# Optimization experiments

Measured on AMD Instinct MI355X. Metric: run time of the kernel, lower is better.

## Reference

```python
import jax, jax.numpy as jnp
import numpy as np

N_E = 1024      # nconcepts (codebook size)
E_DIM = 64      # cdim (codebook vector dim)
BETA = 0.25
LEGACY = True


def setup_inputs() -> dict:
    key = jax.random.key(0)
    k1, k2, k3 = jax.random.split(key, 3)
    z_ = jax.random.normal(k1, (32, 256, 32, 32), jnp.float32)
    # 1x1 conv dis_modulator: 256 -> 64 channels (stored as [out, in])
    conv_w = jax.random.normal(k2, (64, 256), jnp.float32) / np.sqrt(256.0)
    conv_b = jnp.zeros((64,), jnp.float32)
    # embedding.weight.data.uniform_(-1/n_e, 1/n_e)
    emb = jax.random.uniform(k3, (N_E, E_DIM), jnp.float32, -1.0 / N_E, 1.0 / N_E)
    return {"z_": z_, "conv_w": conv_w, "conv_b": conv_b, "emb": emb}


def _forward(z_, conv_w, conv_b, emb):
    sg = jax.lax.stop_gradient
    # dis_modulator: 1x1 conv == per-pixel linear map  (B,Cin,H,W)->(B,Cout,H,W)
    z = jnp.einsum('bchw,oc->bohw', z_, conv_w) + conv_b[None, :, None, None]
    B = z.shape[0]
    # torch .view(-1, e_dim): row-major flatten of (B,C,H,W) into chunks of e_dim
    zf = z.reshape(-1, E_DIM)  # [B*C*H*W/e_dim, e_dim]

    # contrastive term: mean pairwise cosine similarity of codebook rows
    d1 = emb @ emb.T                                  # [n_e, n_e]
    norms = jnp.linalg.norm(emb, axis=1)              # [n_e]
    cosine = d1 / (norms[:, None] * norms[None, :])
    contrastive = jnp.mean(cosine)

    # squared L2 distances: ||z||^2 + ||e||^2 - 2 z.e
    d = (jnp.sum(zf * zf, axis=1, keepdims=True)
         + jnp.sum(emb * emb, axis=1)[None, :]
         - 2.0 * (zf @ emb.T))                        # [N, n_e]
    idx = jnp.argmin(d, axis=1)                       # [N]
    z_q = emb[idx].reshape(z.shape)

    if LEGACY:
        loss = jnp.mean((sg(z_q) - z) ** 2) + BETA * jnp.mean((z_q - sg(z)) ** 2)
    else:
        loss = BETA * jnp.mean((sg(z_q) - z) ** 2) + jnp.mean((z_q - sg(z)) ** 2)
    # hessian_penalty(G, z_, G_z=z): G is an affine 1x1 conv, so the central
    # second difference G(z+x) - 2G(z) + G(z-x) is identically zero -> penalty = 0.
    loss = loss + contrastive

    # straight-through estimator
    z_q_st = z + sg(z_q - z)

    # replicate source exactly: flat zeros(B*n_e) scattered at codebook indices
    sampled = jnp.zeros((B * N_E,), z.dtype).at[idx].set(1.0).reshape(B, N_E)
    min_idx = idx.reshape(B, -1)
    return z_q_st, loss, sampled, min_idx


def reference(z_, conv_w, conv_b, emb):
    z_q, loss, sampled, min_idx = _forward(z_, conv_w, conv_b, emb)
    return z_q, loss, sampled, min_idx
```

## Files before the change

### kernel.cpp

```cpp
#include <hip/hip_runtime.h>
#include <hip/hip_bf16.h>

#define BATCH   32
#define CIN     256
#define COUT    64
#define HW      1024
#define NE      1024
#define ED      64
#define NROW    32768
#define ZTOT    2097152

#define OFF_LOSS 2097152
#define OFF_SAMP 2097153
#define OFF_IDX  2129921

#define XSTR 68
#define ESTR 132

__global__ __launch_bounds__(256) void k_init(float* __restrict__ out_samp,
                                              const float* __restrict__ emb,
                                              float* __restrict__ enorm,
                                              float* __restrict__ invn) {
    int b = blockIdx.x;
    if (b < 128) {
        int i = b * 256 + threadIdx.x;
        out_samp[i] = 0.0f;
    } else {
        int j = (b - 128) * 256 + threadIdx.x;
        const float* e = emb + j * ED;
        float r8[8];
        #pragma unroll
        for (int s = 0; s < 8; s++) { float x = e[s]; r8[s] = x * x; }
        #pragma unroll
        for (int m = 1; m < 8; m++) {
            #pragma unroll
            for (int s = 0; s < 8; s++) { float x = e[8 * m + s]; r8[s] += x * x; }
        }
        float en = ((r8[0] + r8[1]) + (r8[2] + r8[3])) + ((r8[4] + r8[5]) + (r8[6] + r8[7]));
        enorm[j] = en;
        invn[j]  = 1.0f / sqrtf(en);
    }
}

__global__ __launch_bounds__(256) void k_contrast(const float* __restrict__ emb,
                                                  const float* __restrict__ invn,
                                                  float* __restrict__ cpart) {
    int t = threadIdx.x;
    int b = blockIdx.x;
    int d = t & 63, q = t >> 6;
    int i0 = b * 64;
    float s = 0.0f;
    #pragma unroll
    for (int m = 0; m < 16; m++) {
        int i = i0 + q + 4 * m;
        s = fmaf(emb[i * ED + d], invn[i], s);
    }
    __shared__ float S[256];
    S[t] = s;
    __syncthreads();
    if (t < 64)
        cpart[b * 64 + t] = (S[t] + S[t + 64]) + (S[t + 128] + S[t + 192]);
}

__global__ __launch_bounds__(256) void k_conv(const float* __restrict__ x,
                                              const float* __restrict__ w,
                                              const float* __restrict__ bias,
                                              float* __restrict__ z) {
    __shared__ float Xs[64 * XSTR];
    __shared__ float Ws[64 * XSTR];
    int t  = threadIdx.x;
    int b  = blockIdx.y;
    int p0 = blockIdx.x * 64;
    int pg = t & 15;
    int og = t >> 4;
    float acc[4][4];
    #pragma unroll
    for (int i = 0; i < 4; i++)
        #pragma unroll
        for (int j = 0; j < 4; j++) acc[i][j] = 0.0f;

    for (int c0 = 0; c0 < CIN; c0 += 64) {
        __syncthreads();
        {
            int u = t & 15, cg2 = t >> 4;
            #pragma unroll
            for (int m = 0; m < 4; m++) {
                int c = cg2 + 16 * m;
                float4 v = *(const float4*)&x[(size_t)(b * CIN + c0 + c) * HW + p0 + 4 * u];
                *(float4*)&Xs[c * XSTR + 4 * u] = v;
            }
            #pragma unroll
            for (int m = 0; m < 4; m++) {
                int o = cg2 + 16 * m;
                float4 v = *(const float4*)&w[o * CIN + c0 + 4 * u];
                Ws[(4 * u + 0) * XSTR + o] = v.x;
                Ws[(4 * u + 1) * XSTR + o] = v.y;
                Ws[(4 * u + 2) * XSTR + o] = v.z;
                Ws[(4 * u + 3) * XSTR + o] = v.w;
            }
        }
        __syncthreads();
        #pragma unroll 8
        for (int k = 0; k < 64; k++) {
            float4 xv = *(const float4*)&Xs[k * XSTR + 4 * pg];
            float4 wv = *(const float4*)&Ws[k * XSTR + 4 * og];
            float xa[4] = {xv.x, xv.y, xv.z, xv.w};
            float wb[4] = {wv.x, wv.y, wv.z, wv.w};
            #pragma unroll
            for (int i = 0; i < 4; i++)
                #pragma unroll
                for (int j = 0; j < 4; j++)
                    acc[i][j] = fmaf(xa[i], wb[j], acc[i][j]);
        }
    }
    #pragma unroll
    for (int j = 0; j < 4; j++) {
        int o = 4 * og + j;
        float bv = bias[o];
        float4 out;
        out.x = acc[0][j] + bv;
        out.y = acc[1][j] + bv;
        out.z = acc[2][j] + bv;
        out.w = acc[3][j] + bv;
        *(float4*)&z[(size_t)(b * COUT + o) * HW + p0 + 4 * pg] = out;
    }
}

__global__ __launch_bounds__(256) void k_dist(const float* __restrict__ z,
                                              const float* __restrict__ emb,
                                              const float* __restrict__ enorm,
                                              float* __restrict__ out_idx,
                                              float* __restrict__ out_samp,
                                              float* __restrict__ out_zq,
                                              float* __restrict__ ssep) {
    __shared__ float zs[64 * XSTR];
    __shared__ float es[64 * ESTR];
    __shared__ float zn_s[64];
    __shared__ float en_s[128];
    __shared__ float redd_s[16 * 64];
    __shared__ int   redj_s[16 * 64];
    __shared__ int   bj_s[64];
    __shared__ float warr[4];
    int t = threadIdx.x;
    int row0 = blockIdx.x * 64;
    int rg = t & 15;
    int cg = t >> 4;

    {
        int k = t & 63, wv = t >> 6;
        #pragma unroll
        for (int m = 0; m < 4; m++) {
            int v = wv + 4 * m;
            float4 val;
            val.x = z[(size_t)(row0 + 4 * v + 0) * ED + k];
            val.y = z[(size_t)(row0 + 4 * v + 1) * ED + k];
            val.z = z[(size_t)(row0 + 4 * v + 2) * ED + k];
            val.w = z[(size_t)(row0 + 4 * v + 3) * ED + k];
            *(float4*)&zs[k * XSTR + 4 * v] = val;
        }
    }
    if (t < 64) {
        const float* zr = z + (size_t)(row0 + t) * ED;
        float r8[8];
        #pragma unroll
        for (int s = 0; s < 8; s++) { float xx = zr[s]; r8[s] = xx * xx; }
        #pragma unroll
        for (int m = 1; m < 8; m++) {
            #pragma unroll
            for (int s = 0; s < 8; s++) { float xx = zr[8 * m + s]; r8[s] += xx * xx; }
        }
        zn_s[t] = ((r8[0] + r8[1]) + (r8[2] + r8[3])) + ((r8[4] + r8[5]) + (r8[6] + r8[7]));
    }

    float bestd[4];
    int   bestj[4];
    #pragma unroll
    for (int i = 0; i < 4; i++) { bestd[i] = __builtin_huge_valf(); bestj[i] = 0; }

    for (int ch = 0; ch < 8; ch++) {
        int c0 = ch * 128;
        __syncthreads();
        {
            int k = t & 63, wv = t >> 6;
            #pragma unroll
            for (int m = 0; m < 8; m++) {
                int v = wv + 4 * m;
                float4 val;
                val.x = emb[(size_t)(c0 + 4 * v + 0) * ED + k];
                val.y = emb[(size_t)(c0 + 4 * v + 1) * ED + k];
                val.z = emb[(size_t)(c0 + 4 * v + 2) * ED + k];
                val.w = emb[(size_t)(c0 + 4 * v + 3) * ED + k];
                *(float4*)&es[k * ESTR + 4 * v] = val;
            }
            if (t < 32) {
                float4 ev4 = *(const float4*)&enorm[c0 + 4 * t];
                *(float4*)&en_s[4 * t] = ev4;
            }
        }
        __syncthreads();

        float acc[4][8];
        #pragma unroll
        for (int i = 0; i < 4; i++)
            #pragma unroll
            for (int j = 0; j < 8; j++) acc[i][j] = 0.0f;

        #pragma unroll 8
        for (int k = 0; k < 64; k++) {
            float4 xv = *(const float4*)&zs[k * XSTR + 4 * rg];
            float4 e0 = *(const float4*)&es[k * ESTR + 8 * cg];
            float4 e1 = *(const float4*)&es[k * ESTR + 8 * cg + 4];
            float xa[4] = {xv.x, xv.y, xv.z, xv.w};
            float eb[8] = {e0.x, e0.y, e0.z, e0.w, e1.x, e1.y, e1.z, e1.w};
            #pragma unroll
            for (int i = 0; i < 4; i++)
                #pragma unroll
                for (int j = 0; j < 8; j++)
                    acc[i][j] = fmaf(xa[i], eb[j], acc[i][j]);
        }

        #pragma unroll
        for (int i = 0; i < 4; i++) {
            float zn = zn_s[4 * rg + i];
            #pragma unroll
            for (int j = 0; j < 8; j++) {
                int cl = 8 * cg + j;
                float A = zn + en_s[cl];
                float D = A - 2.0f * acc[i][j];
                if (D < bestd[i]) { bestd[i] = D; bestj[i] = c0 + cl; }
            }
        }
    }

    #pragma unroll
    for (int i = 0; i < 4; i++) {
        redd_s[cg * 64 + 4 * rg + i] = bestd[i];
        redj_s[cg * 64 + 4 * rg + i] = bestj[i];
    }
    __syncthreads();
    if (t < 64) {
        float bd = __builtin_huge_valf();
        int   bj = 0x7fffffff;
        #pragma unroll
        for (int c = 0; c < 16; c++) {
            float dd = redd_s[c * 64 + t];
            int   jj = redj_s[c * 64 + t];
            if (dd < bd || (dd == bd && jj < bj)) { bd = dd; bj = jj; }
        }
        int rowg = row0 + t;
        bj_s[t]       = bj;
        out_idx[rowg] = (float)bj;
        atomicExch(&out_samp[bj], 1.0f);
    }
    __syncthreads();

    {
        int r  = t & 63;
        int kq = t >> 6;
        int bj = bj_s[r];
        const float* er = emb + (size_t)bj * ED + kq * 16;
        float sq = 0.0f;
        #pragma unroll
        for (int m = 0; m < 4; m++) {
            float4 ev = *(const float4*)&er[4 * m];
            float zv0 = zs[(kq * 16 + 4 * m + 0) * XSTR + r];
            float zv1 = zs[(kq * 16 + 4 * m + 1) * XSTR + r];
            float zv2 = zs[(kq * 16 + 4 * m + 2) * XSTR + r];
            float zv3 = zs[(kq * 16 + 4 * m + 3) * XSTR + r];
            float d0 = ev.x - zv0, d1 = ev.y - zv1, d2 = ev.z - zv2, d3 = ev.w - zv3;
            float4 o4;
            o4.x = zv0 + d0; o4.y = zv1 + d1; o4.z = zv2 + d2; o4.w = zv3 + d3;
            *(float4*)&out_zq[(size_t)(row0 + r) * ED + kq * 16 + 4 * m] = o4;
            sq += d0 * d0; sq += d1 * d1; sq += d2 * d2; sq += d3 * d3;
        }
        #pragma unroll
        for (int off = 32; off > 0; off >>= 1) sq += __shfl_down(sq, off, 64);
        int lane = t & 63, wv = t >> 6;
        if (lane == 0) warr[wv] = sq;
    }
    __syncthreads();
    if (t == 0)
        ssep[blockIdx.x] = (warr[0] + warr[1]) + (warr[2] + warr[3]);
}

__global__ __launch_bounds__(256) void k_final(const float* __restrict__ ssep,
                                               const float* __restrict__ cpart,
                                               float* __restrict__ out_loss) {
    __shared__ double SD[256];
    __shared__ float  CS;
    int t = threadIdx.x;
    SD[t] = (double)ssep[t] + (double)ssep[t + 256];
    __syncthreads();
    #pragma unroll
    for (int off = 128; off > 0; off >>= 1) {
        if (t < off) SD[t] += SD[t + off];
        __syncthreads();
    }
    if (t < 64) {
        float v = 0.0f;
        #pragma unroll
        for (int m = 0; m < 16; m++) v += cpart[m * 64 + t];
        float sq = v * v;
        #pragma unroll
        for (int off = 32; off > 0; off >>= 1) sq += __shfl_down(sq, off, 64);
        if (t == 0) CS = sq / (1024.0f * 1024.0f);
    }
    __syncthreads();
    if (t == 0) {
        float m = (float)(SD[0] / (double)ZTOT);
        float loss = m + 0.25f * m;
        out_loss[0] = loss + CS;
    }
}

extern "C" void kernel_launch(void* const* d_in, const int* in_sizes, int n_in,
                              void* d_out, int out_size, void* d_ws, size_t ws_size,
                              hipStream_t stream) {
    (void)in_sizes; (void)n_in; (void)out_size; (void)ws_size;
    const float* z_     = (const float*)d_in[0];
    const float* conv_w = (const float*)d_in[1];
    const float* conv_b = (const float*)d_in[2];
    const float* emb    = (const float*)d_in[3];

    float* out      = (float*)d_out;
    float* out_zq   = out;
    float* out_loss = out + OFF_LOSS;
    float* out_samp = out + OFF_SAMP;
    float* out_idx  = out + OFF_IDX;

    char*  ws       = (char*)d_ws;
    float* wz       = (float*)ws;
    float* enorm    = (float*)(ws + 8388608);
    float* invn     = enorm + 1024;
    float* cpart    = (float*)(ws + 8396800);
    float* ssep     = (float*)(ws + 8400896);

    k_init    <<<132, 256, 0, stream>>>(out_samp, emb, enorm, invn);
    k_contrast<<<16,  256, 0, stream>>>(emb, invn, cpart);
    k_conv    <<<dim3(16, 32), 256, 0, stream>>>(z_, conv_w, conv_b, wz);
    k_dist    <<<512, 256, 0, stream>>>(wz, emb, enorm, out_idx, out_samp, out_zq, ssep);
    k_final   <<<1, 256, 0, stream>>>(ssep, cpart, out_loss);
}
```

Before: 166.4 us.

## Restructure distance kernel to read codebook from global and fuse prep kernels

The distance kernel stops staging codebook chunks in shared memory. Each thread now computes an 8x8 register tile, reading codebook vectors straight from global or cache as float4, and z is kept row-major in shared memory with an XOR swizzle. This removes the per-chunk shared-memory fills and barriers, but adds more global and L2 codebook traffic and register pressure (launch bounds now ask for 2 blocks). Separately, the norm and contrastive kernels are merged into one prep kernel, saving a launch.

```diff
diff --git a/kernel.cpp b/kernel.cpp
--- a/kernel.cpp
+++ b/kernel.cpp
@@ -1,65 +1,58 @@
 #include <hip/hip_runtime.h>
 #include <hip/hip_bf16.h>
 
-#define BATCH   32
+#define NE      1024
+#define ED      64
+#define ZTOT    2097152
 #define CIN     256
 #define COUT    64
 #define HW      1024
-#define NE      1024
-#define ED      64
-#define NROW    32768
-#define ZTOT    2097152
 
 #define OFF_LOSS 2097152
 #define OFF_SAMP 2097153
 #define OFF_IDX  2129921
 
 #define XSTR 68
-#define ESTR 132
-
-__global__ __launch_bounds__(256) void k_init(float* __restrict__ out_samp,
+
+__global__ __launch_bounds__(256) void k_prep(float* __restrict__ out_samp,
                                               const float* __restrict__ emb,
                                               float* __restrict__ enorm,
-                                              float* __restrict__ invn) {
-    int b = blockIdx.x;
-    if (b < 128) {
-        int i = b * 256 + threadIdx.x;
-        out_samp[i] = 0.0f;
-    } else {
-        int j = (b - 128) * 256 + threadIdx.x;
-        const float* e = emb + j * ED;
+                                              float* __restrict__ cpart) {
+    int bid = blockIdx.x, t = threadIdx.x;
+    if (bid < 128) {
+        out_samp[bid * 256 + t] = 0.0f;
+        return;
+    }
+    int g = bid - 128;
+    __shared__ float inv_s[64];
+    __shared__ float S[256];
+    if (t < 64) {
+        int j = g * 64 + t;
+        const float* e = emb + (size_t)j * ED;
         float r8[8];
         #pragma unroll
-        for (int s = 0; s < 8; s++) { float x = e[s]; r8[s] = x * x; }
+        for (int s = 0; s < 8; s++) { float v = e[s]; r8[s] = v * v; }
         #pragma unroll
         for (int m = 1; m < 8; m++) {
             #pragma unroll
-            for (int s = 0; s < 8; s++) { float x = e[8 * m + s]; r8[s] += x * x; }
+            for (int s = 0; s < 8; s++) { float v = e[8 * m + s]; r8[s] += v * v; }
         }
         float en = ((r8[0] + r8[1]) + (r8[2] + r8[3])) + ((r8[4] + r8[5]) + (r8[6] + r8[7]));
         enorm[j] = en;
-        invn[j]  = 1.0f / sqrtf(en);
-    }
-}
-
-__global__ __launch_bounds__(256) void k_contrast(const float* __restrict__ emb,
-                                                  const float* __restrict__ invn,
-                                                  float* __restrict__ cpart) {
-    int t = threadIdx.x;
-    int b = blockIdx.x;
+        inv_s[t] = 1.0f / sqrtf(en);
+    }
+    __syncthreads();
     int d = t & 63, q = t >> 6;
-    int i0 = b * 64;
     float s = 0.0f;
     #pragma unroll
     for (int m = 0; m < 16; m++) {
-        int i = i0 + q + 4 * m;
-        s = fmaf(emb[i * ED + d], invn[i], s);
-    }
-    __shared__ float S[256];
+        int i = q + 4 * m;
+        s = fmaf(emb[(size_t)(g * 64 + i) * ED + d], inv_s[i], s);
+    }
     S[t] = s;
     __syncthreads();
     if (t < 64)
-        cpart[b * 64 + t] = (S[t] + S[t + 64]) + (S[t + 128] + S[t + 192]);
+        cpart[g * 64 + t] = (S[t] + S[t + 64]) + (S[t + 128] + S[t + 192]);
 }
 
 __global__ __launch_bounds__(256) void k_conv(const float* __restrict__ x,
@@ -117,139 +110,122 @@
     for (int j = 0; j < 4; j++) {
         int o = 4 * og + j;
         float bv = bias[o];
-        float4 out;
-        out.x = acc[0][j] + bv;
-        out.y = acc[1][j] + bv;
-        out.z = acc[2][j] + bv;
-        out.w = acc[3][j] + bv;
-        *(float4*)&z[(size_t)(b * COUT + o) * HW + p0 + 4 * pg] = out;
-    }
-}
-
-__global__ __launch_bounds__(256) void k_dist(const float* __restrict__ z,
-                                              const float* __restrict__ emb,
-                                              const float* __restrict__ enorm,
-                                              float* __restrict__ out_idx,
-                                              float* __restrict__ out_samp,
-                                              float* __restrict__ out_zq,
-                                              float* __restrict__ ssep) {
-    __shared__ float zs[64 * XSTR];
-    __shared__ float es[64 * ESTR];
+        float4 outv;
+        outv.x = acc[0][j] + bv;
+        outv.y = acc[1][j] + bv;
+        outv.z = acc[2][j] + bv;
+        outv.w = acc[3][j] + bv;
+        *(float4*)&z[(size_t)(b * COUT + o) * HW + p0 + 4 * pg] = outv;
+    }
+}
+
+__global__ __launch_bounds__(256, 2) void k_dist(const float* __restrict__ z,
+                                                 const float* __restrict__ emb,
+                                                 const float* __restrict__ enorm,
+                                                 float* __restrict__ out_idx,
+                                                 float* __restrict__ out_samp,
+                                                 float* __restrict__ out_zq,
+                                                 float* __restrict__ ssep) {
+    __shared__ float zs[64 * 64];
     __shared__ float zn_s[64];
-    __shared__ float en_s[128];
-    __shared__ float redd_s[16 * 64];
-    __shared__ int   redj_s[16 * 64];
+    __shared__ float redd[32 * 64];
+    __shared__ int   redj[32 * 64];
     __shared__ int   bj_s[64];
     __shared__ float warr[4];
-    int t = threadIdx.x;
+    int t    = threadIdx.x;
     int row0 = blockIdx.x * 64;
-    int rg = t & 15;
-    int cg = t >> 4;
+    int rg   = t & 7;
+    int cg   = t >> 3;
 
     {
-        int k = t & 63, wv = t >> 6;
+        int kb = t & 15, rr0 = t >> 4;
         #pragma unroll
         for (int m = 0; m < 4; m++) {
-            int v = wv + 4 * m;
-            float4 val;
-            val.x = z[(size_t)(row0 + 4 * v + 0) * ED + k];
-            val.y = z[(size_t)(row0 + 4 * v + 1) * ED + k];
-            val.z = z[(size_t)(row0 + 4 * v + 2) * ED + k];
-            val.w = z[(size_t)(row0 + 4 * v + 3) * ED + k];
-            *(float4*)&zs[k * XSTR + 4 * v] = val;
+            int rr = rr0 + 16 * m;
+            float4 v = *(const float4*)&z[(size_t)(row0 + rr) * 64 + 4 * kb];
+            *(float4*)&zs[rr * 64 + 4 * (kb ^ (rr & 15))] = v;
         }
     }
     if (t < 64) {
-        const float* zr = z + (size_t)(row0 + t) * ED;
+        const float* zr = z + (size_t)(row0 + t) * 64;
         float r8[8];
         #pragma unroll
-        for (int s = 0; s < 8; s++) { float xx = zr[s]; r8[s] = xx * xx; }
+        for (int s = 0; s < 8; s++) { float v = zr[s]; r8[s] = v * v; }
         #pragma unroll
         for (int m = 1; m < 8; m++) {
             #pragma unroll
-            for (int s = 0; s < 8; s++) { float xx = zr[8 * m + s]; r8[s] += xx * xx; }
+            for (int s = 0; s < 8; s++) { float v = zr[8 * m + s]; r8[s] += v * v; }
         }
         zn_s[t] = ((r8[0] + r8[1]) + (r8[2] + r8[3])) + ((r8[4] + r8[5]) + (r8[6] + r8[7]));
     }
-
-    float bestd[4];
-    int   bestj[4];
-    #pragma unroll
-    for (int i = 0; i < 4; i++) { bestd[i] = __builtin_huge_valf(); bestj[i] = 0; }
-
-    for (int ch = 0; ch < 8; ch++) {
-        int c0 = ch * 128;
-        __syncthreads();
-        {
-            int k = t & 63, wv = t >> 6;
-            #pragma unroll
-            for (int m = 0; m < 8; m++) {
-                int v = wv + 4 * m;
-                float4 val;
-                val.x = emb[(size_t)(c0 + 4 * v + 0) * ED + k];
-                val.y = emb[(size_t)(c0 + 4 * v + 1) * ED + k];
-                val.z = emb[(size_t)(c0 + 4 * v + 2) * ED + k];
-                val.w = emb[(size_t)(c0 + 4 * v + 3) * ED + k];
-                *(float4*)&es[k * ESTR + 4 * v] = val;
-            }
-            if (t < 32) {
-                float4 ev4 = *(const float4*)&enorm[c0 + 4 * t];
-                *(float4*)&en_s[4 * t] = ev4;
-            }
-        }
-        __syncthreads();
-
-        float acc[4][8];
-        #pragma unroll
-        for (int i = 0; i < 4; i++)
+    __syncthreads();
+
+    float znr[8];
+    #pragma unroll
+    for (int i = 0; i < 8; i++) znr[i] = zn_s[rg + 8 * i];
+
+    float bestd[8];
+    int   bestj[8];
+    #pragma unroll
+    for (int i = 0; i < 8; i++) { bestd[i] = __builtin_huge_valf(); bestj[i] = 0; }
+
+    for (int pass = 0; pass < 4; pass++) {
+        float acc[8][8];
+        #pragma unroll
+        for (int i = 0; i < 8; i++)
             #pragma unroll
             for (int j = 0; j < 8; j++) acc[i][j] = 0.0f;
 
-        #pragma unroll 8
-        for (int k = 0; k < 64; k++) {
-            float4 xv = *(const float4*)&zs[k * XSTR + 4 * rg];
-            float4 e0 = *(const float4*)&es[k * ESTR + 8 * cg];
-            float4 e1 = *(const float4*)&es[k * ESTR + 8 * cg + 4];
-            float xa[4] = {xv.x, xv.y, xv.z, xv.w};
-            float eb[8] = {e0.x, e0.y, e0.z, e0.w, e1.x, e1.y, e1.z, e1.w};
-            #pragma unroll
-            for (int i = 0; i < 4; i++)
+        const float* ebase = emb + ((size_t)(pass * 256 + cg) << 6);
+        for (int kb = 0; kb < 16; kb++) {
+            float4 za[8];
+            #pragma unroll
+            for (int i = 0; i < 8; i++) {
+                int rr = rg + 8 * i;
+                za[i] = *(const float4*)&zs[rr * 64 + 4 * (kb ^ (rr & 15))];
+            }
+            #pragma unroll
+            for (int j = 0; j < 8; j++) {
+                float4 ev = *(const float4*)&ebase[((size_t)(32 * j) << 6) + 4 * kb];
                 #pragma unroll
-                for (int j = 0; j < 8; j++)
-                    acc[i][j] = fmaf(xa[i], eb[j], acc[i][j]);
-        }
-
-        #pragma unroll
-        for (int i = 0; i < 4; i++) {
-            float zn = zn_s[4 * rg + i];
-            #pragma unroll
-            for (int j = 0; j < 8; j++) {
-                int cl = 8 * cg + j;
-                float A = zn + en_s[cl];
+                for (int i = 0; i < 8; i++) {
+                    acc[i][j] = fmaf(za[i].x, ev.x, acc[i][j]);
+                    acc[i][j] = fmaf(za[i].y, ev.y, acc[i][j]);
+                    acc[i][j] = fmaf(za[i].z, ev.z, acc[i][j]);
+                    acc[i][j] = fmaf(za[i].w, ev.w, acc[i][j]);
+                }
+            }
+        }
+        #pragma unroll
+        for (int j = 0; j < 8; j++) {
+            int c = pass * 256 + cg + 32 * j;
+            float en = enorm[c];
+            #pragma unroll
+            for (int i = 0; i < 8; i++) {
+                float A = znr[i] + en;
                 float D = A - 2.0f * acc[i][j];
-                if (D < bestd[i]) { bestd[i] = D; bestj[i] = c0 + cl; }
-            }
-        }
-    }
-
-    #pragma unroll
-    for (int i = 0; i < 4; i++) {
-        redd_s[cg * 64 + 4 * rg + i] = bestd[i];
-        redj_s[cg * 64 + 4 * rg + i] = bestj[i];
+                if (D < bestd[i]) { bestd[i] = D; bestj[i] = c; }
+            }
+        }
+    }
+
+    #pragma unroll
+    for (int i = 0; i < 8; i++) {
+        redd[cg * 64 + rg + 8 * i] = bestd[i];
+        redj[cg * 64 + rg + 8 * i] = bestj[i];
     }
     __syncthreads();
     if (t < 64) {
         float bd = __builtin_huge_valf();
         int   bj = 0x7fffffff;
         #pragma unroll
-        for (int c = 0; c < 16; c++) {
-            float dd = redd_s[c * 64 + t];
-            int   jj = redj_s[c * 64 + t];
+        for (int c = 0; c < 32; c++) {
+            float dd = redd[c * 64 + t];
+            int   jj = redj[c * 64 + t];
             if (dd < bd || (dd == bd && jj < bj)) { bd = dd; bj = jj; }
         }
-        int rowg = row0 + t;
-        bj_s[t]       = bj;
-        out_idx[rowg] = (float)bj;
+        bj_s[t] = bj;
+        out_idx[row0 + t] = (float)bj;
         atomicExch(&out_samp[bj], 1.0f);
     }
     __syncthreads();
@@ -258,25 +234,22 @@
         int r  = t & 63;
         int kq = t >> 6;
         int bj = bj_s[r];
-        const float* er = emb + (size_t)bj * ED + kq * 16;
+        const float* er = emb + ((size_t)bj << 6) + kq * 16;
         float sq = 0.0f;
         #pragma unroll
         for (int m = 0; m < 4; m++) {
+            int kb = 4 * kq + m;
+            float4 zv = *(const float4*)&zs[r * 64 + 4 * (kb ^ (r & 15))];
             float4 ev = *(const float4*)&er[4 * m];
-            float zv0 = zs[(kq * 16 + 4 * m + 0) * XSTR + r];
-            float zv1 = zs[(kq * 16 + 4 * m + 1) * XSTR + r];
-            float zv2 = zs[(kq * 16 + 4 * m + 2) * XSTR + r];
-            float zv3 = zs[(kq * 16 + 4 * m + 3) * XSTR + r];
-            float d0 = ev.x - zv0, d1 = ev.y - zv1, d2 = ev.z - zv2, d3 = ev.w - zv3;
+            float d0 = ev.x - zv.x, d1 = ev.y - zv.y, d2 = ev.z - zv.z, d3 = ev.w - zv.w;
             float4 o4;
-            o4.x = zv0 + d0; o4.y = zv1 + d1; o4.z = zv2 + d2; o4.w = zv3 + d3;
-            *(float4*)&out_zq[(size_t)(row0 + r) * ED + kq * 16 + 4 * m] = o4;
+            o4.x = zv.x + d0; o4.y = zv.y + d1; o4.z = zv.z + d2; o4.w = zv.w + d3;
+            *(float4*)&out_zq[((size_t)(row0 + r) << 6) + 4 * kb] = o4;
             sq += d0 * d0; sq += d1 * d1; sq += d2 * d2; sq += d3 * d3;
         }
         #pragma unroll
         for (int off = 32; off > 0; off >>= 1) sq += __shfl_down(sq, off, 64);
-        int lane = t & 63, wv = t >> 6;
-        if (lane == 0) warr[wv] = sq;
+        if ((t & 63) == 0) warr[t >> 6] = sq;
     }
     __syncthreads();
     if (t == 0)
@@ -308,8 +281,7 @@
     __syncthreads();
     if (t == 0) {
         float m = (float)(SD[0] / (double)ZTOT);
-        float loss = m + 0.25f * m;
-        out_loss[0] = loss + CS;
+        out_loss[0] = (m + 0.25f * m) + CS;
     }
 }
 
@@ -328,16 +300,14 @@
     float* out_samp = out + OFF_SAMP;
     float* out_idx  = out + OFF_IDX;
 
-    char*  ws       = (char*)d_ws;
-    float* wz       = (float*)ws;
-    float* enorm    = (float*)(ws + 8388608);
-    float* invn     = enorm + 1024;
-    float* cpart    = (float*)(ws + 8396800);
-    float* ssep     = (float*)(ws + 8400896);
-
-    k_init    <<<132, 256, 0, stream>>>(out_samp, emb, enorm, invn);
-    k_contrast<<<16,  256, 0, stream>>>(emb, invn, cpart);
-    k_conv    <<<dim3(16, 32), 256, 0, stream>>>(z_, conv_w, conv_b, wz);
-    k_dist    <<<512, 256, 0, stream>>>(wz, emb, enorm, out_idx, out_samp, out_zq, ssep);
-    k_final   <<<1, 256, 0, stream>>>(ssep, cpart, out_loss);
-}
+    char*   ws    = (char*)d_ws;
+    float*  wz    = (float*)ws;
+    float*  enorm = (float*)(ws + 8388608);
+    float*  cpart = enorm + 1024;
+    float*  ssep  = cpart + 1024;
+
+    k_prep <<<144, 256, 0, stream>>>(out_samp, emb, enorm, cpart);
+    k_conv <<<dim3(16, 32), 256, 0, stream>>>(z_, conv_w, conv_b, wz);
+    k_dist <<<512, 256, 0, stream>>>(wz, emb, enorm, out_idx, out_samp, out_zq, ssep);
+    k_final<<<1, 256, 0, stream>>>(ssep, cpart, out_loss);
+}
```

New measurement: 181.5 us. 9.1% more time.
